# Kernel tuning notes

Hardware: AMD Instinct MI355X
Metric: run time of the kernel (lower is better)

The kernel has to match this reference:

```python
import jax, jax.numpy as jnp
import numpy as np

B, F, N, S, D = 128, 3, 64, 96, 64  # batch, features, nodes, steps, d_model
DIN = F + 1  # delta_t channel appended inside forward


def _layer_norm(x, g, b, eps=1e-5):
    mu = jnp.mean(x, -1, keepdims=True)
    var = jnp.mean((x - mu) ** 2, -1, keepdims=True)
    return (x - mu) * jax.lax.rsqrt(var + eps) * g + b


def _encoder_layer(x, inw, inb, ow, ob, w1, b1, w2, b2, g1, be1, g2, be2):
    # x: (B, N, D). Torch post-norm TransformerEncoderLayer, nhead=1, eval mode (no dropout).
    q, k, v = jnp.split(x @ inw.T + inb, 3, axis=-1)
    scores = jnp.einsum('bnd,bmd->bnm', q, k) / jnp.sqrt(jnp.asarray(D, x.dtype))
    a = jnp.einsum('bnm,bmd->bnd', jax.nn.softmax(scores, -1), v) @ ow.T + ob
    x = _layer_norm(x + a, g1, be1)
    ff = jax.nn.relu(x @ w1.T + b1) @ w2.T + b2
    return _layer_norm(x + ff, g2, be2)


def _diff_conv(x, adj, w, b):
    x1 = jnp.einsum('bcv,wv->bcw', x, adj)
    x2 = jnp.einsum('bcv,wv->bcw', x1, adj)
    z = jnp.concatenate([x, x1, x2], axis=1)  # (B, 3C, N)
    return jnp.einsum('bcn,oc->bon', z, w) + b[None, :, None]


def _forward(x, adj, h0, tp, uw, ub, cw, cb):
    times = x[:, 2, 0, :]  # (B, S) timestamps
    dt = jnp.concatenate([jnp.zeros((B, 1), x.dtype), times[:, 1:] - times[:, :-1]], axis=1)  # (B, S)
    xs = (jnp.transpose(x, (3, 0, 1, 2)), jnp.transpose(dt)[:, :, None])  # (S,B,F,N), (S,B,1)

    def step(h, inp):
        xt, d = inp  # (B,F,N), (B,1)
        xin = jnp.concatenate([xt, jnp.broadcast_to(d[:, :, None], (B, 1, N))], axis=1)  # (B,DIN,N)
        y = jnp.transpose(h, (0, 2, 1))  # (B, N, D): nodes are the attention sequence
        for i in range(2):
            y = _encoder_layer(y, *(a[i] for a in tp))
        eps = jnp.transpose(y, (0, 2, 1))  # (B, D, N)
        hd = jnp.sqrt(1.0 - d)[:, :, None] * h - jnp.sqrt(d)[:, :, None] * eps
        xg = jnp.concatenate([xin, hd], axis=1)  # (B, DIN+D, N)
        u = jax.nn.sigmoid(_diff_conv(xg, adj, uw, ub))
        c = jnp.tanh(_diff_conv(xg, adj, cw, cb))
        hn = u * hd + (1.0 - u) * c
        return hn, hn

    _, outs = jax.lax.scan(step, h0, xs)  # (S, B, D, N)
    return jnp.transpose(outs, (1, 3, 2, 0))  # (B, N, D, S) == stack().permute(1,3,2,0)


def setup_inputs() -> dict:
    key = jax.random.key(0)
    ks = jax.random.split(key, 12)
    s = 0.05
    x = jax.random.normal(ks[0], (B, F, N, S), jnp.float32)
    inc = jax.random.uniform(ks[1], (B, S), jnp.float32, 0.001, 0.01)
    x = x.at[:, 2, 0, :].set(jnp.cumsum(inc, axis=1))  # monotone times, delta_t in (0, 0.01)
    adj = jax.random.uniform(ks[2], (N, N), jnp.float32)
    adj = adj / jnp.sum(adj, axis=1, keepdims=True)
    h0 = jax.random.normal(ks[3], (B, D, N), jnp.float32)
    lengths = jax.random.randint(ks[4], (B,), 1, S, jnp.int32)  # unused by forward
    return {
        'x': x, 'adj': adj, 'lengths': lengths, 'h0': h0,
        't_inw': jax.random.normal(ks[5], (2, 3 * D, D), jnp.float32) * s,
        't_inb': jnp.zeros((2, 3 * D), jnp.float32),
        't_ow': jax.random.normal(ks[6], (2, D, D), jnp.float32) * s,
        't_ob': jnp.zeros((2, D), jnp.float32),
        't_w1': jax.random.normal(ks[7], (2, 64, D), jnp.float32) * s,
        't_b1': jnp.zeros((2, 64), jnp.float32),
        't_w2': jax.random.normal(ks[8], (2, D, 64), jnp.float32) * s,
        't_b2': jnp.zeros((2, D), jnp.float32),
        't_g1': jnp.ones((2, D), jnp.float32), 't_be1': jnp.zeros((2, D), jnp.float32),
        't_g2': jnp.ones((2, D), jnp.float32), 't_be2': jnp.zeros((2, D), jnp.float32),
        'uw': jax.random.normal(ks[9], (D, 3 * (DIN + D)), jnp.float32) * s,
        'ub': jnp.zeros((D,), jnp.float32),
        'cw': jax.random.normal(ks[10], (D, 3 * (DIN + D)), jnp.float32) * s,
        'cb': jnp.zeros((D,), jnp.float32),
    }


def reference(x, adj, lengths, h0, t_inw, t_inb, t_ow, t_ob, t_w1, t_b1, t_w2, t_b2,
              t_g1, t_be1, t_g2, t_be2, uw, ub, cw, cb):
    tp = (t_inw, t_inb, t_ow, t_ob, t_w1, t_b1, t_w2, t_b2, t_g1, t_be1, t_g2, t_be2)
    return _forward(x, adj, h0, tp, uw, ub, cw, cb)
```

## Files before the change

### kernel.cpp

```cpp
#include <hip/hip_runtime.h>
#include <math.h>

#define TPB 512

typedef __attribute__((ext_vector_type(8))) short bf16x8;
typedef __attribute__((ext_vector_type(4))) float f32x4;
typedef unsigned short u16;

#define MFMA(a, b, c) __builtin_amdgcn_mfma_f32_16x16x32_bf16(a, b, c, 0, 0, 0)

__device__ __forceinline__ u16 f2bf(float f) {
  union { float f; unsigned u; } v; v.f = f;
  unsigned u = v.u;
  return (u16)((u + 0x7fffu + ((u >> 16) & 1u)) >> 16);
}
__device__ __forceinline__ float bf2f(u16 h) {
  union { unsigned u; float f; } v; v.u = ((unsigned)h) << 16; return v.f;
}
__device__ __forceinline__ unsigned cvt2(float a0, float a1) {
  return (unsigned)f2bf(a0) | ((unsigned)f2bf(a1) << 16);
}
__device__ __forceinline__ void cvt4u(float a0, float a1, float a2, float a3, u16 o[4]) {
  o[0] = f2bf(a0); o[1] = f2bf(a1); o[2] = f2bf(a2); o[3] = f2bf(a3);
}
// ... 12 lines not shown
}
template<int PREW>
__device__ __forceinline__ bf16x8 wfrag(const float* __restrict__ Wg,
                                        const u16* __restrict__ Wp,
                                        int m, int f, int kh, int lane) {
  if constexpr (PREW)
    return *(const bf16x8*)(Wp + (size_t)m * 4096 + f * 1024 + kh * 512 + lane * 8);
  else
    return fragG(Wg, f * 16, 64, kh * 32, lane);
}

__global__ __launch_bounds__(256)
void prep_kernel(const float* __restrict__ t_inw, const float* __restrict__ t_ow,
                 const float* __restrict__ t_w1, const float* __restrict__ t_w2,
                 const float* __restrict__ adj, const float* __restrict__ x,
                 u16* __restrict__ wp, float* __restrict__ adj2,
                 float* __restrict__ wsDT, u16* __restrict__ wsX, int doX) {
  int m = blockIdx.x;
  if (m == 12) {
    for (int e = threadIdx.x; e < 4096; e += 256) {
      int w = e >> 6, u = e & 63;
      float sum = 0.f;
      for (int v = 0; v < 64; ++v) sum += adj[w * 64 + v] * adj[v * 64 + u];
      adj2[e] = sum;
    }
    return;
  }
  if (m >= 13) {
    if (!doX) return;
    int b = m - 13;
    const float* times = x + ((size_t)b * 3 + 2) * 64 * 96;
    for (int i = threadIdx.x; i < 96 * 256; i += 256) {
      int s = i >> 8, idx = i & 255, f = idx >> 6, n = idx & 63;
      float v;
      if (f < 3) v = x[(((size_t)b * 3 + f) * 64 + n) * 96 + s];
      else {
        float dt = s ? (times[s] - times[s - 1]) : 0.f;
        v = dt;
        if (n == 0) wsDT[b * 96 + s] = dt;
      }
      wsX[((size_t)b * 96 + s) * 256 + idx] = f2bf(v);
    }
    return;
  }
  int l = m / 6, r = m % 6;
  const float* W;
  if (r < 3)       W = t_inw + l * 12288 + r * 4096;
  else if (r == 3) W = t_ow + l * 4096;
  else if (r == 4) W = t_w1 + l * 4096;
  else             W = t_w2 + l * 4096;
  for (int t = threadIdx.x; t < 4096; t += 256) {
    int j = t & 7, ln = (t >> 3) & 63, kh = (t >> 9) & 1, f = t >> 10;
    int row = f * 16 + (ln & 15);
    int k = kh * 32 + ((ln >> 4) << 3) + j;
    wp[(size_t)m * 4096 + t] = f2bf(W[row * 64 + k]);
  }
}

template<int PREW>
__global__ __launch_bounds__(TPB, 2)
void gcrnn_kernel(const float* __restrict__ x,
                  const float* __restrict__ adj,
                  const float* __restrict__ h0,
                  const float* __restrict__ t_inw, const float* __restrict__ t_inb,
                  const float* __restrict__ t_ow,  const float* __restrict__ t_ob,
                  const float* __restrict__ t_w1,  const float* __restrict__ t_b1,
                  const float* __restrict__ t_w2,  const float* __restrict__ t_b2,
                  const float* __restrict__ t_g1,  const float* __restrict__ t_be1,
                  const float* __restrict__ t_g2,  const float* __restrict__ t_be2,
                  const float* __restrict__ uw,    const float* __restrict__ ub,
                  const float* __restrict__ cw,    const float* __restrict__ cb,
                  const u16* __restrict__ wsW,
                  const float* __restrict__ adj2g,
                  const float* __restrict__ wsDT,
                  const u16* __restrict__ wsX,
                  float* __restrict__ wsOut,
                  float* __restrict__ out,
                  int useStage, int useXT)
{
  const int b = blockIdx.x;
  const int tid = threadIdx.x;
  const int wv = tid >> 6;
  const int lane = tid & 63;
  const int lx = lane & 15;
  const int gq = (lane >> 4) << 2;
  const int rs = wv & 3;
  const int of0 = (wv >> 2) * 2;
  const int fA = wv >> 2;

  __shared__ __align__(16) u16 adjB[64 * 72];
  __shared__ __align__(16) u16 adj2B[64 * 72];
  __shared__ __align__(16) u16 ysB[64 * 72];
  __shared__ __align__(16) u16 pool[4 * 4608];
  __shared__ __align__(16) u16 zTB[64 * 232];
  __shared__ __align__(16) u16 uwcwB[2 * 4 * 7 * 512];

  u16* Qb  = pool;
  u16* Kb  = pool + 4608;
  u16* VTb = pool + 9216;
  u16* Pb  = pool + 13824;
  u16* xgB = pool;

  float hreg[2][4];
  {
    const int nb = rs * 16 + gq;
#pragma unroll
    for (int ff = 0; ff < 2; ++ff) {
      int o = (of0 + ff) * 16 + lx;
      float4 hv = *(const float4*)(h0 + (size_t)b * 4096 + o * 64 + nb);
#pragma unroll
      for (int j = 0; j < 4; ++j) {
        hreg[ff][j] = (&hv.x)[j];
        ysB[(nb + j) * 72 + o] = f2bf(hreg[ff][j]);
      }
    }
  }
  for (int i = tid; i < 4096; i += TPB)
    adjB[(i >> 6) * 72 + (i & 63)] = f2bf(adj[i]);
  if constexpr (PREW) {
    for (int i = tid; i < 4096; i += TPB)
      adj2B[(i >> 6) * 72 + (i & 63)] = f2bf(adj2g[i]);
  } else {
    for (int i = tid; i < 4096; i += TPB) {
      int w = i >> 6, u = i & 63;
      float sum = 0.f;
      for (int v = 0; v < 64; ++v) sum += adj[w * 64 + v] * adj[v * 64 + u];
      adj2B[w * 72 + u] = f2bf(sum);
    }
  }
  for (int i = tid; i < 2 * 4 * 7 * 512; i += TPB) {
    int t = i;
    int j = t & 7; t >>= 3;
    int ln = t & 63; t >>= 6;
    int kh = t % 7; t /= 7;
    int f = t & 3; int mat = t >> 2;
    int o = f * 16 + (ln & 15);
    int k = kh * 32 + ((ln >> 4) << 3) + j;
    const float* W = mat ? cw : uw;
    uwcwB[i] = (k < 204) ? f2bf(W[o * 204 + k]) : (u16)0;
  }
  for (int i = tid; i < 64 * 28; i += TPB)
    zTB[(i / 28) * 232 + 204 + (i % 28)] = 0;
  __syncthreads();

  const float* times = x + ((size_t)b * 3 + 2) * 64 * 96;
  float hdreg[2][4];

  for (int s = 0; s < 96; ++s) {
    float dcur = useXT ? wsDT[b * 96 + s]
                       : ((s == 0) ? 0.f : (times[s] - times[s - 1]));
    float sq1 = sqrtf(1.f - dcur), sq2 = sqrtf(dcur);

    for (int l = 0; l < 2; ++l) {
      const int l6 = l * 6;
      const float* inw = t_inw + l * 12288;
      const float* inb = t_inb + l * 192;
      const float* ow  = t_ow  + l * 4096;
      const float* ob  = t_ob  + l * 64;
      const float* w1  = t_w1  + l * 4096;
      const float* bb1 = t_b1  + l * 64;
      const float* w2  = t_w2  + l * 4096;
      const float* bb2 = t_b2  + l * 64;
      const float* g1  = t_g1  + l * 64;
      const float* be1 = t_be1 + l * 64;
      const float* g2  = t_g2  + l * 64;
      const float* be2 = t_be2 + l * 64;

      bf16x8 fq[2][2], fk[2][2], fw1r[2][2], fvr[2];
#pragma unroll
      for (int fi = 0; fi < 2; ++fi)
#pragma unroll
        for (int kh = 0; kh < 2; ++kh) {
          fq[fi][kh]   = wfrag<PREW>(inw,        wsW, l6 + 0, fA + fi * 2, kh, lane);
          fk[fi][kh]   = wfrag<PREW>(inw + 4096, wsW, l6 + 1, fA + fi * 2, kh, lane);
          fw1r[fi][kh] = wfrag<PREW>(w1,         wsW, l6 + 4, fA + fi * 2, kh, lane);
        }
      if (wv >= 4) {
#pragma unroll
        for (int kh = 0; kh < 2; ++kh)
          fvr[kh] = wfrag<PREW>(inw + 8192, wsW, l6 + 2, rs, kh, lane);
      }

      {
        bf16x8 a0 = fragL(ysB, rs * 16, 72, 0, lane);
        bf16x8 a1 = fragL(ysB, rs * 16, 72, 32, lane);
#pragma unroll
        for (int fi = 0; fi < 2; ++fi) {
          int f = fA + fi * 2;
          int col = f * 16 + lx;
          {
            f32x4 acc = {0.f, 0.f, 0.f, 0.f};
            acc = MFMA(a0, fq[fi][0], acc);
            acc = MFMA(a1, fq[fi][1], acc);
            float bv = inb[col];
            u16 o4[4]; cvt4u(acc[0] + bv, acc[1] + bv, acc[2] + bv, acc[3] + bv, o4);
#pragma unroll
            for (int j = 0; j < 4; ++j)
              Qb[(rs * 16 + gq + j) * 72 + col] = o4[j];
          }
          {
// ... 35 lines not shown
          for (int f = 0; f < 4; ++f) { float e = __expf(sc[f][j] - m1); sc[f][j] = e; s1 += e; }
          s1 += __shfl_xor(s1, 1); s1 += __shfl_xor(s1, 2);
          s1 += __shfl_xor(s1, 4); s1 += __shfl_xor(s1, 8);
          float inv = 1.f / s1;
          int row = rs * 16 + gq + j;
          u16 o4[4];
          cvt4u(sc[0][j] * inv, sc[1][j] * inv, sc[2][j] * inv, sc[3][j] * inv, o4);
#pragma unroll
          for (int f = 0; f < 4; ++f)
            Pb[row * 72 + f * 16 + lx] = o4[f];
        }
      } else {
#pragma unroll
        for (int f = 0; f < 4; ++f) {
          f32x4 acc = {0.f, 0.f, 0.f, 0.f};
          acc = MFMA(fvr[0], fragL(ysB, f * 16, 72, 0, lane), acc);
          acc = MFMA(fvr[1], fragL(ysB, f * 16, 72, 32, lane), acc);
          int dd0 = rs * 16 + gq;
          u16 o4[4];
          cvt4u(acc[0] + inb[128 + dd0], acc[1] + inb[128 + dd0 + 1],
                acc[2] + inb[128 + dd0 + 2], acc[3] + inb[128 + dd0 + 3], o4);
#pragma unroll
          for (int j = 0; j < 4; ++j)
            VTb[(dd0 + j) * 72 + f * 16 + lx] = o4[j];
        }
      }
      __syncthreads();

      bf16x8 fo[4][2];
      if (wv < 4) {
#pragma unroll
        for (int f = 0; f < 4; ++f)
#pragma unroll
          for (int kh = 0; kh < 2; ++kh)
            fo[f][kh] = wfrag<PREW>(ow, wsW, l6 + 3, f, kh, lane);
      }
      {
        bf16x8 pa0 = fragL(Pb, rs * 16, 72, 0, lane);
        bf16x8 pa1 = fragL(Pb, rs * 16, 72, 32, lane);
#pragma unroll
        for (int fi = 0; fi < 2; ++fi) {
          int f = fA + fi * 2;
          f32x4 acc = {0.f, 0.f, 0.f, 0.f};
          acc = MFMA(pa0, fragL(VTb, f * 16, 72, 0, lane), acc);
          acc = MFMA(pa1, fragL(VTb, f * 16, 72, 32, lane), acc);
          u16 o4[4]; cvt4u(acc[0], acc[1], acc[2], acc[3], o4);
#pragma unroll
          for (int j = 0; j < 4; ++j)
            Qb[(rs * 16 + gq + j) * 72 + f * 16 + lx] = o4[j];
        }
// ... 2 lines not shown

      if (wv < 4) {
        bf16x8 a0 = fragL(Qb, rs * 16, 72, 0, lane);
        bf16x8 a1 = fragL(Qb, rs * 16, 72, 32, lane);
        float t4[4][4];
#pragma unroll
        for (int f = 0; f < 4; ++f) {
          f32x4 acc = {0.f, 0.f, 0.f, 0.f};
          acc = MFMA(a0, fo[f][0], acc);
          acc = MFMA(a1, fo[f][1], acc);
          int col = f * 16 + lx;
          float bv = ob[col];
#pragma unroll
          for (int j = 0; j < 4; ++j) {
            int row = rs * 16 + gq + j;
            t4[f][j] = acc[j] + bv + bf2f(ysB[row * 72 + col]);
          }
        }
#pragma unroll
        for (int j = 0; j < 4; ++j) {
          float s1 = t4[0][j] + t4[1][j] + t4[2][j] + t4[3][j];
          float s2 = t4[0][j] * t4[0][j] + t4[1][j] * t4[1][j]
                   + t4[2][j] * t4[2][j] + t4[3][j] * t4[3][j];
          s1 += __shfl_xor(s1, 1); s2 += __shfl_xor(s2, 1);
          s1 += __shfl_xor(s1, 2); s2 += __shfl_xor(s2, 2);
          s1 += __shfl_xor(s1, 4); s2 += __shfl_xor(s2, 4);
          s1 += __shfl_xor(s1, 8); s2 += __shfl_xor(s2, 8);
          float mu = s1 * 0.015625f;
          float rstd = rsqrtf(s2 * 0.015625f - mu * mu + 1e-5f);
          int row = rs * 16 + gq + j;
          u16 o4[4];
          cvt4u((t4[0][j] - mu) * rstd * g1[0 * 16 + lx] + be1[0 * 16 + lx],
                (t4[1][j] - mu) * rstd * g1[1 * 16 + lx] + be1[1 * 16 + lx],
                (t4[2][j] - mu) * rstd * g1[2 * 16 + lx] + be1[2 * 16 + lx],
                (t4[3][j] - mu) * rstd * g1[3 * 16 + lx] + be1[3 * 16 + lx], o4);
#pragma unroll
          for (int f = 0; f < 4; ++f)
            ysB[row * 72 + f * 16 + lx] = o4[f];
        }
      }
      __syncthreads();

      bf16x8 fw2[4][2];
      if (wv < 4) {
#pragma unroll
        for (int f = 0; f < 4; ++f)
#pragma unroll
          for (int kh = 0; kh < 2; ++kh)
            fw2[f][kh] = wfrag<PREW>(w2, wsW, l6 + 5, f, kh, lane);
      }
      {
        bf16x8 a0 = fragL(ysB, rs * 16, 72, 0, lane);
        bf16x8 a1 = fragL(ysB, rs * 16, 72, 32, lane);
#pragma unroll
        for (int fi = 0; fi < 2; ++fi) {
          int f = fA + fi * 2;
          f32x4 acc = {0.f, 0.f, 0.f, 0.f};
          acc = MFMA(a0, fw1r[fi][0], acc);
          acc = MFMA(a1, fw1r[fi][1], acc);
          int col = f * 16 + lx;
          float bv = bb1[col];
          u16 o4[4];
          cvt4u(fmaxf(acc[0] + bv, 0.f), fmaxf(acc[1] + bv, 0.f),
                fmaxf(acc[2] + bv, 0.f), fmaxf(acc[3] + bv, 0.f), o4);
#pragma unroll
          for (int j = 0; j < 4; ++j)
            Kb[(rs * 16 + gq + j) * 72 + col] = o4[j];
        }
      }
      __syncthreads();

      if (wv < 4) {
        bf16x8 a0 = fragL(Kb, rs * 16, 72, 0, lane);
        bf16x8 a1 = fragL(Kb, rs * 16, 72, 32, lane);
        float t4[4][4];
#pragma unroll
        for (int f = 0; f < 4; ++f) {
          f32x4 acc = {0.f, 0.f, 0.f, 0.f};
          acc = MFMA(a0, fw2[f][0], acc);
          acc = MFMA(a1, fw2[f][1], acc);
          int col = f * 16 + lx;
          float bv = bb2[col];
#pragma unroll
          for (int j = 0; j < 4; ++j) {
            int row = rs * 16 + gq + j;
            t4[f][j] = acc[j] + bv + bf2f(ysB[row * 72 + col]);
          }
        }
#pragma unroll
        for (int j = 0; j < 4; ++j) {
          float s1 = t4[0][j] + t4[1][j] + t4[2][j] + t4[3][j];
          float s2 = t4[0][j] * t4[0][j] + t4[1][j] * t4[1][j]
                   + t4[2][j] * t4[2][j] + t4[3][j] * t4[3][j];
          s1 += __shfl_xor(s1, 1); s2 += __shfl_xor(s2, 1);
          s1 += __shfl_xor(s1, 2); s2 += __shfl_xor(s2, 2);
// ... 4 lines not shown
          int row = rs * 16 + gq + j;
          u16 o4[4];
          cvt4u((t4[0][j] - mu) * rstd * g2[0 * 16 + lx] + be2[0 * 16 + lx],
                (t4[1][j] - mu) * rstd * g2[1 * 16 + lx] + be2[1 * 16 + lx],
                (t4[2][j] - mu) * rstd * g2[2 * 16 + lx] + be2[2 * 16 + lx],
                (t4[3][j] - mu) * rstd * g2[3 * 16 + lx] + be2[3 * 16 + lx], o4);
#pragma unroll
          for (int f = 0; f < 4; ++f)
            ysB[row * 72 + f * 16 + lx] = o4[f];
        }
      }
      __syncthreads();
    }

    {
      if (useXT) {
        const u16* xr = wsX + ((size_t)b * 96 + s) * 256;
        for (int i = tid; i < 256; i += TPB) {
          u16 v = xr[i];
          int f = i >> 6, n = i & 63;
          xgB[f * 72 + n] = v;
          zTB[n * 232 + f] = v;
        }
      } else {
        for (int i = tid; i < 256; i += TPB) {
          int f = i >> 6, n = i & 63;
          float v = (f < 3) ? x[(((size_t)b * 3 + f) * 64 + n) * 96 + s] : dcur;
          u16 v16 = f2bf(v);
          xgB[f * 72 + n] = v16;
          zTB[n * 232 + f] = v16;
        }
      }
      const int nb = rs * 16 + gq;
#pragma unroll
      for (int ff = 0; ff < 2; ++ff) {
        int o = (of0 + ff) * 16 + lx;
        float hd0 = sq1 * hreg[ff][0] - sq2 * bf2f(ysB[(nb + 0) * 72 + o]);
        float hd1 = sq1 * hreg[ff][1] - sq2 * bf2f(ysB[(nb + 1) * 72 + o]);
        float hd2 = sq1 * hreg[ff][2] - sq2 * bf2f(ysB[(nb + 2) * 72 + o]);
        float hd3 = sq1 * hreg[ff][3] - sq2 * bf2f(ysB[(nb + 3) * 72 + o]);
        hdreg[ff][0] = hd0; hdreg[ff][1] = hd1; hdreg[ff][2] = hd2; hdreg[ff][3] = hd3;
        unsigned p0 = cvt2(hd0, hd1), p1 = cvt2(hd2, hd3);
        zTB[(nb + 0) * 232 + 4 + o] = (u16)p0;
        zTB[(nb + 1) * 232 + 4 + o] = (u16)(p0 >> 16);
        zTB[(nb + 2) * 232 + 4 + o] = (u16)p1;
        zTB[(nb + 3) * 232 + 4 + o] = (u16)(p1 >> 16);
// ... 46 lines not shown
        for (int j = 0; j < 4; ++j) {
          float u = 1.f / (1.f + __expf(-(aU[ff][j] + bu_)));
          float z = aC[ff][j] + bc_;
          z = fminf(fmaxf(z, -15.f), 15.f);
          float e2 = __expf(2.f * z);
          float cval = (e2 - 1.f) / (e2 + 1.f);
          float hn = u * hdreg[ff][j] + (1.f - u) * cval;
          hreg[ff][j] = hn;
          (&ov.x)[j] = hn;
        }
        unsigned pk0 = cvt2(ov.x, ov.y), pk1 = cvt2(ov.z, ov.w);
        ysB[(nb + 0) * 72 + o] = (u16)pk0;
        ysB[(nb + 1) * 72 + o] = (u16)(pk0 >> 16);
        ysB[(nb + 2) * 72 + o] = (u16)pk1;
        ysB[(nb + 3) * 72 + o] = (u16)(pk1 >> 16);
        if (useStage) {
          *(float4*)(wsOut + ((size_t)b * 96 + s) * 4096 + o * 64 + nb) = ov;
        } else {
#pragma unroll
          for (int j = 0; j < 4; ++j)
            out[((size_t)(b * 64 + (nb + j)) * 64 + o) * 96 + s] = (&ov.x)[j];
        }
      }
    }
    __syncthreads();
  }
}

__global__ __launch_bounds__(256)
void transp_kernel(const float* __restrict__ ws, float* __restrict__ out) {
  int blk = blockIdx.x;
  int b = blk >> 6, o = blk & 63;
  __shared__ float t[96 * 68];
  for (int i = threadIdx.x; i < 96 * 64; i += 256) {
    int ss = i >> 6, n = i & 63;
    t[ss * 68 + n] = ws[((size_t)b * 96 + ss) * 4096 + o * 64 + n];
  }
// ... 18 lines not shown
  const float* t_ob  = (const float*)d_in[7];
  const float* t_w1  = (const float*)d_in[8];
  const float* t_b1  = (const float*)d_in[9];
  const float* t_w2  = (const float*)d_in[10];
  const float* t_b2  = (const float*)d_in[11];
  const float* t_g1  = (const float*)d_in[12];
  const float* t_be1 = (const float*)d_in[13];
  const float* t_g2  = (const float*)d_in[14];
  const float* t_be2 = (const float*)d_in[15];
  const float* uw    = (const float*)d_in[16];
  const float* ub    = (const float*)d_in[17];
  const float* cw    = (const float*)d_in[18];
  const float* cb    = (const float*)d_in[19];
  float* out = (float*)d_out;

  const size_t offAdj2 = 98304;
  const size_t offDT   = 114688;
  const size_t offX    = 163840;
  const size_t offStageFull = 6455296;
  const size_t stageBytes = (size_t)128 * 96 * 4096 * 4;

  int prew = 0, useStage = 0, useXT = 0;
  size_t stageOff = 0;
  if (ws_size >= offStageFull + stageBytes) { prew = 1; useXT = 1; useStage = 1; stageOff = offStageFull; }
  else if (ws_size >= offX + stageBytes)    { prew = 1; useStage = 1; stageOff = offX; }
  else if (ws_size >= stageBytes)           { useStage = 1; }
  else if (ws_size >= offX)                 { prew = 1; }

  u16*   wsW   = (u16*)d_ws;
  float* adj2g = (float*)((char*)d_ws + offAdj2);
  float* wsDT  = (float*)((char*)d_ws + offDT);
  u16*   wsX   = (u16*)((char*)d_ws + offX);
  float* wsOut = (float*)((char*)d_ws + stageOff);

  if (prew)
    hipLaunchKernelGGL(prep_kernel, dim3(13 + (useXT ? 128 : 0)), dim3(256), 0, stream,
                       t_inw, t_ow, t_w1, t_w2, adj, x, wsW, adj2g, wsDT, wsX, useXT);

  if (prew)
    hipLaunchKernelGGL(gcrnn_kernel<1>, dim3(128), dim3(TPB), 0, stream,
                       x, adj, h0, t_inw, t_inb, t_ow, t_ob, t_w1, t_b1,
                       t_w2, t_b2, t_g1, t_be1, t_g2, t_be2, uw, ub, cw, cb,
                       wsW, adj2g, wsDT, wsX, wsOut, out, useStage, useXT);
  else
    hipLaunchKernelGGL(gcrnn_kernel<0>, dim3(128), dim3(TPB), 0, stream,
                       x, adj, h0, t_inw, t_inb, t_ow, t_ob, t_w1, t_b1,
                       t_w2, t_b2, t_g1, t_be1, t_g2, t_be2, uw, ub, cw, cb,
                       wsW, adj2g, wsDT, wsX, wsOut, out, useStage, 0);

  if (useStage)
    hipLaunchKernelGGL(transp_kernel, dim3(128 * 64), dim3(256), 0, stream, wsOut, out);
}
```

Measured before the change: 1.599 ms.

## Split fast path with double-buffered LDS, fused FFN/diffusion stages and pre-swizzled adj²

Splits the kernel into a fast path, used when workspace is large enough, and a separate fallback kernel. The fast path gives Q/K/V/P/xg their own LDS buffers and ping-pongs the layer input between Y0 and Y1 to remove aliasing. It also folds the last layer's FFN/LayerNorm epilogue straight into the hd/xg build, and interleaves the first diffusion hops with the gate MFMAs. adj² is precomputed and pre-swizzled into MFMA fragment layout in global memory, and biases are hoisted out of the step loop. The aim is fewer barriers and less per-step LDS/global traffic, at the cost of more LDS and register pressure, which may reduce occupancy.

```diff
diff --git a/kernel.cpp b/kernel.cpp
--- a/kernel.cpp
+++ b/kernel.cpp
@@ -50,20 +50,27 @@
 void prep_kernel(const float* __restrict__ t_inw, const float* __restrict__ t_ow,
                  const float* __restrict__ t_w1, const float* __restrict__ t_w2,
                  const float* __restrict__ adj, const float* __restrict__ x,
-                 u16* __restrict__ wp, float* __restrict__ adj2,
-                 float* __restrict__ wsDT, u16* __restrict__ wsX, int doX) {
+                 u16* __restrict__ wp, u16* __restrict__ wpA2,
+                 float* __restrict__ wsDT, u16* __restrict__ wsX) {
   int m = blockIdx.x;
   if (m == 12) {
+    __shared__ float a2[4096];
     for (int e = threadIdx.x; e < 4096; e += 256) {
       int w = e >> 6, u = e & 63;
       float sum = 0.f;
       for (int v = 0; v < 64; ++v) sum += adj[w * 64 + v] * adj[v * 64 + u];
-      adj2[e] = sum;
+      a2[e] = sum;
+    }
+    __syncthreads();
+    for (int t = threadIdx.x; t < 4096; t += 256) {
+      int j = t & 7, ln = (t >> 3) & 63, kh = (t >> 9) & 1, f = t >> 10;
+      int row = f * 16 + (ln & 15);
+      int k = kh * 32 + ((ln >> 4) << 3) + j;
+      wpA2[t] = f2bf(a2[row * 64 + k]);
     }
     return;
   }
   if (m >= 13) {
-    if (!doX) return;
     int b = m - 13;
     const float* times = x + ((size_t)b * 3 + 2) * 64 * 96;
     for (int i = threadIdx.x; i < 96 * 256; i += 256) {
@@ -93,26 +100,18 @@
   }
 }
 
-template<int PREW>
 __global__ __launch_bounds__(TPB, 2)
-void gcrnn_kernel(const float* __restrict__ x,
-                  const float* __restrict__ adj,
-                  const float* __restrict__ h0,
-                  const float* __restrict__ t_inw, const float* __restrict__ t_inb,
-                  const float* __restrict__ t_ow,  const float* __restrict__ t_ob,
-                  const float* __restrict__ t_w1,  const float* __restrict__ t_b1,
-                  const float* __restrict__ t_w2,  const float* __restrict__ t_b2,
-                  const float* __restrict__ t_g1,  const float* __restrict__ t_be1,
-                  const float* __restrict__ t_g2,  const float* __restrict__ t_be2,
-                  const float* __restrict__ uw,    const float* __restrict__ ub,
-                  const float* __restrict__ cw,    const float* __restrict__ cb,
-                  const u16* __restrict__ wsW,
-                  const float* __restrict__ adj2g,
-                  const float* __restrict__ wsDT,
-                  const u16* __restrict__ wsX,
-                  float* __restrict__ wsOut,
-                  float* __restrict__ out,
-                  int useStage, int useXT)
+void gcrnn_fast(const float* __restrict__ adj,
+                const float* __restrict__ h0,
+                const float* __restrict__ t_inb, const float* __restrict__ t_ob,
+                const float* __restrict__ t_b1,  const float* __restrict__ t_b2,
+                const float* __restrict__ t_g1,  const float* __restrict__ t_be1,
+                const float* __restrict__ t_g2,  const float* __restrict__ t_be2,
+                const float* __restrict__ uw,    const float* __restrict__ ub,
+                const float* __restrict__ cw,    const float* __restrict__ cb,
+                const u16* __restrict__ wsW,  const u16* __restrict__ wsA2,
+                const float* __restrict__ wsDT, const u16* __restrict__ wsX,
+                float* __restrict__ wsOut)
 {
   const int b = blockIdx.x;
   const int tid = threadIdx.x;
@@ -125,17 +124,15 @@
   const int fA = wv >> 2;
 
   __shared__ __align__(16) u16 adjB[64 * 72];
-  __shared__ __align__(16) u16 adj2B[64 * 72];
-  __shared__ __align__(16) u16 ysB[64 * 72];
-  __shared__ __align__(16) u16 pool[4 * 4608];
+  __shared__ __align__(16) u16 Y0[64 * 72];
+  __shared__ __align__(16) u16 Y1[64 * 72];
+  __shared__ __align__(16) u16 Qb[64 * 72];
+  __shared__ __align__(16) u16 Kb[64 * 72];
+  __shared__ __align__(16) u16 VTb[64 * 72];
+  __shared__ __align__(16) u16 Pb[64 * 72];
+  __shared__ __align__(16) u16 xgB[80 * 72];
   __shared__ __align__(16) u16 zTB[64 * 232];
   __shared__ __align__(16) u16 uwcwB[2 * 4 * 7 * 512];
-
-  u16* Qb  = pool;
-  u16* Kb  = pool + 4608;
-  u16* VTb = pool + 9216;
-  u16* Pb  = pool + 13824;
-  u16* xgB = pool;
 
   float hreg[2][4];
   {
@@ -147,23 +144,12 @@
 #pragma unroll
       for (int j = 0; j < 4; ++j) {
         hreg[ff][j] = (&hv.x)[j];
-        ysB[(nb + j) * 72 + o] = f2bf(hreg[ff][j]);
+        Y0[(nb + j) * 72 + o] = f2bf(hreg[ff][j]);
       }
     }
   }
   for (int i = tid; i < 4096; i += TPB)
     adjB[(i >> 6) * 72 + (i & 63)] = f2bf(adj[i]);
-  if constexpr (PREW) {
-    for (int i = tid; i < 4096; i += TPB)
-      adj2B[(i >> 6) * 72 + (i & 63)] = f2bf(adj2g[i]);
-  } else {
-    for (int i = tid; i < 4096; i += TPB) {
-      int w = i >> 6, u = i & 63;
-      float sum = 0.f;
-      for (int v = 0; v < 64; ++v) sum += adj[w * 64 + v] * adj[v * 64 + u];
-      adj2B[w * 72 + u] = f2bf(sum);
-    }
-  }
   for (int i = tid; i < 2 * 4 * 7 * 512; i += TPB) {
     int t = i;
     int j = t & 7; t >>= 3;
@@ -177,25 +163,23 @@
   }
   for (int i = tid; i < 64 * 28; i += TPB)
     zTB[(i / 28) * 232 + 204 + (i % 28)] = 0;
+  for (int i = tid; i < 12 * 72; i += TPB)
+    xgB[68 * 72 + i] = 0;
   __syncthreads();
 
-  const float* times = x + ((size_t)b * 3 + 2) * 64 * 96;
+  const float buo = ub[of0 * 16 + lx], buo2 = ub[(of0 + 1) * 16 + lx];
+  const float bco = cb[of0 * 16 + lx], bco2 = cb[(of0 + 1) * 16 + lx];
   float hdreg[2][4];
 
   for (int s = 0; s < 96; ++s) {
-    float dcur = useXT ? wsDT[b * 96 + s]
-                       : ((s == 0) ? 0.f : (times[s] - times[s - 1]));
+    float dcur = wsDT[b * 96 + s];
     float sq1 = sqrtf(1.f - dcur), sq2 = sqrtf(dcur);
 
     for (int l = 0; l < 2; ++l) {
       const int l6 = l * 6;
-      const float* inw = t_inw + l * 12288;
       const float* inb = t_inb + l * 192;
-      const float* ow  = t_ow  + l * 4096;
       const float* ob  = t_ob  + l * 64;
-      const float* w1  = t_w1  + l * 4096;
       const float* bb1 = t_b1  + l * 64;
-      const float* w2  = t_w2  + l * 4096;
       const float* bb2 = t_b2  + l * 64;
       const float* g1  = t_g1  + l * 64;
       const float* be1 = t_be1 + l * 64;
@@ -207,19 +191,19 @@
       for (int fi = 0; fi < 2; ++fi)
 #pragma unroll
         for (int kh = 0; kh < 2; ++kh) {
-          fq[fi][kh]   = wfrag<PREW>(inw,        wsW, l6 + 0, fA + fi * 2, kh, lane);
-          fk[fi][kh]   = wfrag<PREW>(inw + 4096, wsW, l6 + 1, fA + fi * 2, kh, lane);
-          fw1r[fi][kh] = wfrag<PREW>(w1,         wsW, l6 + 4, fA + fi * 2, kh, lane);
+          fq[fi][kh]   = wfrag<1>(nullptr, wsW, l6 + 0, fA + fi * 2, kh, lane);
+          fk[fi][kh]   = wfrag<1>(nullptr, wsW, l6 + 1, fA + fi * 2, kh, lane);
+          fw1r[fi][kh] = wfrag<1>(nullptr, wsW, l6 + 4, fA + fi * 2, kh, lane);
         }
       if (wv >= 4) {
 #pragma unroll
         for (int kh = 0; kh < 2; ++kh)
-          fvr[kh] = wfrag<PREW>(inw + 8192, wsW, l6 + 2, rs, kh, lane);
+          fvr[kh] = wfrag<1>(nullptr, wsW, l6 + 2, rs, kh, lane);
       }
 
       {
-        bf16x8 a0 = fragL(ysB, rs * 16, 72, 0, lane);
-        bf16x8 a1 = fragL(ysB, rs * 16, 72, 32, lane);
+        bf16x8 a0 = fragL(Y0, rs * 16, 72, 0, lane);
+        bf16x8 a1 = fragL(Y0, rs * 16, 72, 32, lane);
 #pragma unroll
         for (int fi = 0; fi < 2; ++fi) {
           int f = fA + fi * 2;
@@ -285,8 +269,8 @@
 #pragma unroll
         for (int f = 0; f < 4; ++f) {
           f32x4 acc = {0.f, 0.f, 0.f, 0.f};
-          acc = MFMA(fvr[0], fragL(ysB, f * 16, 72, 0, lane), acc);
-          acc = MFMA(fvr[1], fragL(ysB, f * 16, 72, 32, lane), acc);
+          acc = MFMA(fvr[0], fragL(Y0, f * 16, 72, 0, lane), acc);
+          acc = MFMA(fvr[1], fragL(Y0, f * 16, 72, 32, lane), acc);
           int dd0 = rs * 16 + gq;
           u16 o4[4];
           cvt4u(acc[0] + inb[128 + dd0], acc[1] + inb[128 + dd0 + 1],
@@ -304,7 +288,7 @@
         for (int f = 0; f < 4; ++f)
 #pragma unroll
           for (int kh = 0; kh < 2; ++kh)
-            fo[f][kh] = wfrag<PREW>(ow, wsW, l6 + 3, f, kh, lane);
+            fo[f][kh] = wfrag<1>(nullptr, wsW, l6 + 3, f, kh, lane);
       }
       {
         bf16x8 pa0 = fragL(Pb, rs * 16, 72, 0, lane);
@@ -337,7 +321,7 @@
 #pragma unroll
           for (int j = 0; j < 4; ++j) {
             int row = rs * 16 + gq + j;
-            t4[f][j] = acc[j] + bv + bf2f(ysB[row * 72 + col]);
+            t4[f][j] = acc[j] + bv + bf2f(Y0[row * 72 + col]);
           }
         }
 #pragma unroll
@@ -359,22 +343,20 @@
                 (t4[3][j] - mu) * rstd * g1[3 * 16 + lx] + be1[3 * 16 + lx], o4);
 #pragma unroll
           for (int f = 0; f < 4; ++f)
-            ysB[row * 72 + f * 16 + lx] = o4[f];
+            Y1[row * 72 + f * 16 + lx] = o4[f];
         }
       }
       __syncthreads();
 
       bf16x8 fw2[4][2];
-      if (wv < 4) {
-#pragma unroll
-        for (int f = 0; f < 4; ++f)
-#pragma unroll
-          for (int kh = 0; kh < 2; ++kh)
-            fw2[f][kh] = wfrag<PREW>(w2, wsW, l6 + 5, f, kh, lane);
-      }
+#pragma unroll
+      for (int f = 0; f < 4; ++f)
+#pragma unroll
+        for (int kh = 0; kh < 2; ++kh)
+          fw2[f][kh] = wfrag<1>(nullptr, wsW, l6 + 5, f, kh, lane);
       {
-        bf16x8 a0 = fragL(ysB, rs * 16, 72, 0, lane);
-        bf16x8 a1 = fragL(ysB, rs * 16, 72, 32, lane);
+        bf16x8 a0 = fragL(Y1, rs * 16, 72, 0, lane);
+        bf16x8 a1 = fragL(Y1, rs * 16, 72, 32, lane);
 #pragma unroll
         for (int fi = 0; fi < 2; ++fi) {
           int f = fA + fi * 2;
@@ -393,6 +375,461 @@
       }
       __syncthreads();
 
+      if (l == 0) {
+        if (wv < 4) {
+          bf16x8 a0 = fragL(Kb, rs * 16, 72, 0, lane);
+          bf16x8 a1 = fragL(Kb, rs * 16, 72, 32, lane);
+          float t4[4][4];
+#pragma unroll
+          for (int f = 0; f < 4; ++f) {
+            f32x4 acc = {0.f, 0.f, 0.f, 0.f};
+            acc = MFMA(a0, fw2[f][0], acc);
+            acc = MFMA(a1, fw2[f][1], acc);
+            int col = f * 16 + lx;
+            float bv = bb2[col];
+#pragma unroll
+            for (int j = 0; j < 4; ++j) {
+              int row = rs * 16 + gq + j;
+              t4[f][j] = acc[j] + bv + bf2f(Y1[row * 72 + col]);
+            }
+          }
+#pragma unroll
+          for (int j = 0; j < 4; ++j) {
+            float s1 = t4[0][j] + t4[1][j] + t4[2][j] + t4[3][j];
+            float s2 = t4[0][j] * t4[0][j] + t4[1][j] * t4[1][j]
+                     + t4[2][j] * t4[2][j] + t4[3][j] * t4[3][j];
+            s1 += __shfl_xor(s1, 1); s2 += __shfl_xor(s2, 1);
+            s1 += __shfl_xor(s1, 2); s2 += __shfl_xor(s2, 2);
+            s1 += __shfl_xor(s1, 4); s2 += __shfl_xor(s2, 4);
+            s1 += __shfl_xor(s1, 8); s2 += __shfl_xor(s2, 8);
+            float mu = s1 * 0.015625f;
+            float rstd = rsqrtf(s2 * 0.015625f - mu * mu + 1e-5f);
+            int row = rs * 16 + gq + j;
+            u16 o4[4];
+            cvt4u((t4[0][j] - mu) * rstd * g2[0 * 16 + lx] + be2[0 * 16 + lx],
+                  (t4[1][j] - mu) * rstd * g2[1 * 16 + lx] + be2[1 * 16 + lx],
+                  (t4[2][j] - mu) * rstd * g2[2 * 16 + lx] + be2[2 * 16 + lx],
+                  (t4[3][j] - mu) * rstd * g2[3 * 16 + lx] + be2[3 * 16 + lx], o4);
+#pragma unroll
+            for (int f = 0; f < 4; ++f)
+              Y0[row * 72 + f * 16 + lx] = o4[f];
+          }
+        }
+      } else {
+        bf16x8 a0 = fragL(Kb, rs * 16, 72, 0, lane);
+        bf16x8 a1 = fragL(Kb, rs * 16, 72, 32, lane);
+        float t4[4][4];
+#pragma unroll
+        for (int f = 0; f < 4; ++f) {
+          f32x4 acc = {0.f, 0.f, 0.f, 0.f};
+          acc = MFMA(a0, fw2[f][0], acc);
+          acc = MFMA(a1, fw2[f][1], acc);
+          int col = f * 16 + lx;
+          float bv = bb2[col];
+#pragma unroll
+          for (int j = 0; j < 4; ++j) {
+            int row = rs * 16 + gq + j;
+            t4[f][j] = acc[j] + bv + bf2f(Y1[row * 72 + col]);
+          }
+        }
+#pragma unroll
+        for (int j = 0; j < 4; ++j) {
+          float s1 = t4[0][j] + t4[1][j] + t4[2][j] + t4[3][j];
+          float s2 = t4[0][j] * t4[0][j] + t4[1][j] * t4[1][j]
+                   + t4[2][j] * t4[2][j] + t4[3][j] * t4[3][j];
+          s1 += __shfl_xor(s1, 1); s2 += __shfl_xor(s2, 1);
+          s1 += __shfl_xor(s1, 2); s2 += __shfl_xor(s2, 2);
+          s1 += __shfl_xor(s1, 4); s2 += __shfl_xor(s2, 4);
+          s1 += __shfl_xor(s1, 8); s2 += __shfl_xor(s2, 8);
+          float mu = s1 * 0.015625f;
+          float rstd = rsqrtf(s2 * 0.015625f - mu * mu + 1e-5f);
+#pragma unroll
+          for (int f = 0; f < 4; ++f) {
+            int col = f * 16 + lx;
+            t4[f][j] = (t4[f][j] - mu) * rstd * g2[col] + be2[col];
+          }
+        }
+        {
+          const u16* xr = wsX + ((size_t)b * 96 + s) * 256;
+          for (int i = tid; i < 256; i += TPB) {
+            u16 v = xr[i];
+            int f = i >> 6, n = i & 63;
+            xgB[f * 72 + n] = v;
+            zTB[n * 232 + f] = v;
+          }
+        }
+        const int nb = rs * 16 + gq;
+#pragma unroll
+        for (int f = 0; f < 4; ++f) {
+          if ((f >> 1) == (wv >> 2)) {
+            const int ff = f & 1;
+            int o = f * 16 + lx;
+            float hd0 = sq1 * hreg[ff][0] - sq2 * t4[f][0];
+            float hd1 = sq1 * hreg[ff][1] - sq2 * t4[f][1];
+            float hd2 = sq1 * hreg[ff][2] - sq2 * t4[f][2];
+            float hd3 = sq1 * hreg[ff][3] - sq2 * t4[f][3];
+            hdreg[ff][0] = hd0; hdreg[ff][1] = hd1;
+            hdreg[ff][2] = hd2; hdreg[ff][3] = hd3;
+            unsigned p0 = cvt2(hd0, hd1), p1 = cvt2(hd2, hd3);
+            zTB[(nb + 0) * 232 + 4 + o] = (u16)p0;
+            zTB[(nb + 1) * 232 + 4 + o] = (u16)(p0 >> 16);
+            zTB[(nb + 2) * 232 + 4 + o] = (u16)p1;
+            zTB[(nb + 3) * 232 + 4 + o] = (u16)(p1 >> 16);
+            uint2 pk; pk.x = p0; pk.y = p1;
+            *(uint2*)(xgB + (4 + o) * 72 + nb) = pk;
+          }
+        }
+      }
+      __syncthreads();
+    }
+
+    f32x4 aU0 = {0.f,0.f,0.f,0.f}, aU1 = {0.f,0.f,0.f,0.f};
+    f32x4 aC0 = {0.f,0.f,0.f,0.f}, aC1 = {0.f,0.f,0.f,0.f};
+    {
+      bf16x8 g0 = *(const bf16x8*)(wsA2 + rs * 1024 + lane * 8);
+      bf16x8 g1 = *(const bf16x8*)(wsA2 + rs * 1024 + 512 + lane * 8);
+      bf16x8 aj0 = fragL(adjB, rs * 16, 72, 0, lane);
+      bf16x8 aj1 = fragL(adjB, rs * 16, 72, 32, lane);
+
+#define HT(A0, A1, CF, OFF) { \
+      f32x4 acc = {0.f,0.f,0.f,0.f}; \
+      acc = MFMA(A0, fragL(xgB, (CF) * 16, 72, 0, lane), acc); \
+      acc = MFMA(A1, fragL(xgB, (CF) * 16, 72, 32, lane), acc); \
+      int c = (CF) * 16 + lx; \
+      if (c < 68) { u16 o4[4]; cvt4u(acc[0], acc[1], acc[2], acc[3], o4); \
+        _Pragma("unroll") for (int j = 0; j < 4; ++j) \
+          zTB[(rs * 16 + gq + j) * 232 + (OFF) + c] = o4[j]; } }
+
+#define J01 { _Pragma("unroll") for (int kh = 0; kh < 2; ++kh) { \
+      bf16x8 a = fragL(zTB, rs * 16, 232, kh * 32, lane); \
+      { const u16* pu = uwcwB + (size_t)((of0 + 0) * 7 + kh) * 512 + lane * 8; \
+        const u16* pc = uwcwB + (size_t)((4 + of0 + 0) * 7 + kh) * 512 + lane * 8; \
+        aU0 = MFMA(a, *(const bf16x8*)pu, aU0); \
+        aC0 = MFMA(a, *(const bf16x8*)pc, aC0); } \
+      { const u16* pu = uwcwB + (size_t)((of0 + 1) * 7 + kh) * 512 + lane * 8; \
+        const u16* pc = uwcwB + (size_t)((4 + of0 + 1) * 7 + kh) * 512 + lane * 8; \
+        aU1 = MFMA(a, *(const bf16x8*)pu, aU1); \
+        aC1 = MFMA(a, *(const bf16x8*)pc, aC1); } } }
+
+      if (wv < 4) {
+        HT(aj0, aj1, 0, 68); HT(aj0, aj1, 2, 68); HT(aj0, aj1, 4, 68);
+        J01;
+        HT(g0, g1, 1, 136); HT(g0, g1, 3, 136);
+      } else {
+        HT(aj0, aj1, 1, 68); HT(aj0, aj1, 3, 68);
+        J01;
+        HT(g0, g1, 0, 136); HT(g0, g1, 2, 136); HT(g0, g1, 4, 136);
+      }
+#undef HT
+#undef J01
+    }
+    __syncthreads();
+
+    {
+#pragma unroll
+      for (int kh = 2; kh < 7; ++kh) {
+        bf16x8 a = fragL(zTB, rs * 16, 232, kh * 32, lane);
+        {
+          const u16* pu = uwcwB + (size_t)((of0 + 0) * 7 + kh) * 512 + lane * 8;
+          const u16* pc = uwcwB + (size_t)((4 + of0 + 0) * 7 + kh) * 512 + lane * 8;
+          aU0 = MFMA(a, *(const bf16x8*)pu, aU0);
+          aC0 = MFMA(a, *(const bf16x8*)pc, aC0);
+        }
+        {
+          const u16* pu = uwcwB + (size_t)((of0 + 1) * 7 + kh) * 512 + lane * 8;
+          const u16* pc = uwcwB + (size_t)((4 + of0 + 1) * 7 + kh) * 512 + lane * 8;
+          aU1 = MFMA(a, *(const bf16x8*)pu, aU1);
+          aC1 = MFMA(a, *(const bf16x8*)pc, aC1);
+        }
+      }
+      const int nb = rs * 16 + gq;
+#pragma unroll
+      for (int ff = 0; ff < 2; ++ff) {
+        f32x4 aU = ff ? aU1 : aU0;
+        f32x4 aC = ff ? aC1 : aC0;
+        float bu_ = ff ? buo2 : buo;
+        float bc_ = ff ? bco2 : bco;
+        int o = (of0 + ff) * 16 + lx;
+        float4 ov;
+#pragma unroll
+        for (int j = 0; j < 4; ++j) {
+          float u = 1.f / (1.f + __expf(-(aU[j] + bu_)));
+          float z = aC[j] + bc_;
+          z = fminf(fmaxf(z, -15.f), 15.f);
+          float e2 = __expf(2.f * z);
+          float cval = (e2 - 1.f) / (e2 + 1.f);
+          float hn = u * hdreg[ff][j] + (1.f - u) * cval;
+          hreg[ff][j] = hn;
+          (&ov.x)[j] = hn;
+        }
+        unsigned pk0 = cvt2(ov.x, ov.y), pk1 = cvt2(ov.z, ov.w);
+        Y0[(nb + 0) * 72 + o] = (u16)pk0;
+        Y0[(nb + 1) * 72 + o] = (u16)(pk0 >> 16);
+        Y0[(nb + 2) * 72 + o] = (u16)pk1;
+        Y0[(nb + 3) * 72 + o] = (u16)(pk1 >> 16);
+        *(float4*)(wsOut + ((size_t)b * 96 + s) * 4096 + o * 64 + nb) = ov;
+      }
+    }
+    __syncthreads();
+  }
+}
+
+__global__ __launch_bounds__(TPB, 2)
+void gcrnn_fb(const float* __restrict__ x, const float* __restrict__ adj,
+              const float* __restrict__ h0,
+              const float* __restrict__ t_inw, const float* __restrict__ t_inb,
+              const float* __restrict__ t_ow,  const float* __restrict__ t_ob,
+              const float* __restrict__ t_w1,  const float* __restrict__ t_b1,
+              const float* __restrict__ t_w2,  const float* __restrict__ t_b2,
+              const float* __restrict__ t_g1,  const float* __restrict__ t_be1,
+              const float* __restrict__ t_g2,  const float* __restrict__ t_be2,
+              const float* __restrict__ uw,    const float* __restrict__ ub,
+              const float* __restrict__ cw,    const float* __restrict__ cb,
+              float* __restrict__ out)
+{
+  const int b = blockIdx.x;
+  const int tid = threadIdx.x;
+  const int wv = tid >> 6;
+  const int lane = tid & 63;
+  const int lx = lane & 15;
+  const int gq = (lane >> 4) << 2;
+  const int rs = wv & 3;
+  const int of0 = (wv >> 2) * 2;
+  const int fA = wv >> 2;
+
+  __shared__ __align__(16) u16 adjB[64 * 72];
+  __shared__ __align__(16) u16 adj2B[64 * 72];
+  __shared__ __align__(16) u16 ysB[64 * 72];
+  __shared__ __align__(16) u16 pool[4 * 4608];
+  __shared__ __align__(16) u16 zTB[64 * 232];
+  __shared__ __align__(16) u16 uwcwB[2 * 4 * 7 * 512];
+
+  u16* Qb  = pool;
+  u16* Kb  = pool + 4608;
+  u16* VTb = pool + 9216;
+  u16* Pb  = pool + 13824;
+  u16* xgB = pool;
+
+  float hreg[2][4];
+  {
+    const int nb = rs * 16 + gq;
+#pragma unroll
+    for (int ff = 0; ff < 2; ++ff) {
+      int o = (of0 + ff) * 16 + lx;
+      float4 hv = *(const float4*)(h0 + (size_t)b * 4096 + o * 64 + nb);
+#pragma unroll
+      for (int j = 0; j < 4; ++j) {
+        hreg[ff][j] = (&hv.x)[j];
+        ysB[(nb + j) * 72 + o] = f2bf(hreg[ff][j]);
+      }
+    }
+  }
+  for (int i = tid; i < 4096; i += TPB)
+    adjB[(i >> 6) * 72 + (i & 63)] = f2bf(adj[i]);
+  for (int i = tid; i < 4096; i += TPB) {
+    int w = i >> 6, u = i & 63;
+    float sum = 0.f;
+    for (int v = 0; v < 64; ++v) sum += adj[w * 64 + v] * adj[v * 64 + u];
+    adj2B[w * 72 + u] = f2bf(sum);
+  }
+  for (int i = tid; i < 2 * 4 * 7 * 512; i += TPB) {
+    int t = i;
+    int j = t & 7; t >>= 3;
+    int ln = t & 63; t >>= 6;
+    int kh = t % 7; t /= 7;
+    int f = t & 3; int mat = t >> 2;
+    int o = f * 16 + (ln & 15);
+    int k = kh * 32 + ((ln >> 4) << 3) + j;
+    const float* W = mat ? cw : uw;
+    uwcwB[i] = (k < 204) ? f2bf(W[o * 204 + k]) : (u16)0;
+  }
+  for (int i = tid; i < 64 * 28; i += TPB)
+    zTB[(i / 28) * 232 + 204 + (i % 28)] = 0;
+  __syncthreads();
+
+  const float* times = x + ((size_t)b * 3 + 2) * 64 * 96;
+  float hdreg[2][4];
+
+  for (int s = 0; s < 96; ++s) {
+    float dcur = (s == 0) ? 0.f : (times[s] - times[s - 1]);
+    float sq1 = sqrtf(1.f - dcur), sq2 = sqrtf(dcur);
+
+    for (int l = 0; l < 2; ++l) {
+      const float* inw = t_inw + l * 12288;
+      const float* inb = t_inb + l * 192;
+      const float* ow  = t_ow  + l * 4096;
+      const float* ob  = t_ob  + l * 64;
+      const float* w1  = t_w1  + l * 4096;
+      const float* bb1 = t_b1  + l * 64;
+      const float* w2  = t_w2  + l * 4096;
+      const float* bb2 = t_b2  + l * 64;
+      const float* g1  = t_g1  + l * 64;
+      const float* be1 = t_be1 + l * 64;
+      const float* g2  = t_g2  + l * 64;
+      const float* be2 = t_be2 + l * 64;
+
+      {
+        bf16x8 a0 = fragL(ysB, rs * 16, 72, 0, lane);
+        bf16x8 a1 = fragL(ysB, rs * 16, 72, 32, lane);
+#pragma unroll
+        for (int fi = 0; fi < 2; ++fi) {
+          int f = fA + fi * 2;
+          int col = f * 16 + lx;
+          {
+            f32x4 acc = {0.f, 0.f, 0.f, 0.f};
+            acc = MFMA(a0, fragG(inw, f * 16, 64, 0, lane), acc);
+            acc = MFMA(a1, fragG(inw, f * 16, 64, 32, lane), acc);
+            float bv = inb[col];
+            u16 o4[4]; cvt4u(acc[0] + bv, acc[1] + bv, acc[2] + bv, acc[3] + bv, o4);
+#pragma unroll
+            for (int j = 0; j < 4; ++j)
+              Qb[(rs * 16 + gq + j) * 72 + col] = o4[j];
+          }
+          {
+            f32x4 acc = {0.f, 0.f, 0.f, 0.f};
+            acc = MFMA(a0, fragG(inw + 4096, f * 16, 64, 0, lane), acc);
+            acc = MFMA(a1, fragG(inw + 4096, f * 16, 64, 32, lane), acc);
+            float bv = inb[64 + col];
+            u16 o4[4]; cvt4u(acc[0] + bv, acc[1] + bv, acc[2] + bv, acc[3] + bv, o4);
+#pragma unroll
+            for (int j = 0; j < 4; ++j)
+              Kb[(rs * 16 + gq + j) * 72 + col] = o4[j];
+          }
+        }
+      }
+      __syncthreads();
+
+      if (wv < 4) {
+        bf16x8 qa0 = fragL(Qb, rs * 16, 72, 0, lane);
+        bf16x8 qa1 = fragL(Qb, rs * 16, 72, 32, lane);
+        f32x4 sc[4];
+#pragma unroll
+        for (int f = 0; f < 4; ++f) {
+          f32x4 acc = {0.f, 0.f, 0.f, 0.f};
+          acc = MFMA(qa0, fragL(Kb, f * 16, 72, 0, lane), acc);
+          acc = MFMA(qa1, fragL(Kb, f * 16, 72, 32, lane), acc);
+#pragma unroll
+          for (int j = 0; j < 4; ++j) acc[j] *= 0.125f;
+          sc[f] = acc;
+        }
+#pragma unroll
+        for (int j = 0; j < 4; ++j) {
+          float m1 = fmaxf(fmaxf(sc[0][j], sc[1][j]), fmaxf(sc[2][j], sc[3][j]));
+          m1 = fmaxf(m1, __shfl_xor(m1, 1));
+          m1 = fmaxf(m1, __shfl_xor(m1, 2));
+          m1 = fmaxf(m1, __shfl_xor(m1, 4));
+          m1 = fmaxf(m1, __shfl_xor(m1, 8));
+          float s1 = 0.f;
+#pragma unroll
+          for (int f = 0; f < 4; ++f) { float e = __expf(sc[f][j] - m1); sc[f][j] = e; s1 += e; }
+          s1 += __shfl_xor(s1, 1); s1 += __shfl_xor(s1, 2);
+          s1 += __shfl_xor(s1, 4); s1 += __shfl_xor(s1, 8);
+          float inv = 1.f / s1;
+          int row = rs * 16 + gq + j;
+          u16 o4[4];
+          cvt4u(sc[0][j] * inv, sc[1][j] * inv, sc[2][j] * inv, sc[3][j] * inv, o4);
+#pragma unroll
+          for (int f = 0; f < 4; ++f)
+            Pb[row * 72 + f * 16 + lx] = o4[f];
+        }
+      } else {
+        bf16x8 wa0 = fragG(inw + 8192, rs * 16, 64, 0, lane);
+        bf16x8 wa1 = fragG(inw + 8192, rs * 16, 64, 32, lane);
+#pragma unroll
+        for (int f = 0; f < 4; ++f) {
+          f32x4 acc = {0.f, 0.f, 0.f, 0.f};
+          acc = MFMA(wa0, fragL(ysB, f * 16, 72, 0, lane), acc);
+          acc = MFMA(wa1, fragL(ysB, f * 16, 72, 32, lane), acc);
+          int dd0 = rs * 16 + gq;
+          u16 o4[4];
+          cvt4u(acc[0] + inb[128 + dd0], acc[1] + inb[128 + dd0 + 1],
+                acc[2] + inb[128 + dd0 + 2], acc[3] + inb[128 + dd0 + 3], o4);
+#pragma unroll
+          for (int j = 0; j < 4; ++j)
+            VTb[(dd0 + j) * 72 + f * 16 + lx] = o4[j];
+        }
+      }
+      __syncthreads();
+
+      {
+        bf16x8 pa0 = fragL(Pb, rs * 16, 72, 0, lane);
+        bf16x8 pa1 = fragL(Pb, rs * 16, 72, 32, lane);
+#pragma unroll
+        for (int fi = 0; fi < 2; ++fi) {
+          int f = fA + fi * 2;
+          f32x4 acc = {0.f, 0.f, 0.f, 0.f};
+          acc = MFMA(pa0, fragL(VTb, f * 16, 72, 0, lane), acc);
+          acc = MFMA(pa1, fragL(VTb, f * 16, 72, 32, lane), acc);
+          u16 o4[4]; cvt4u(acc[0], acc[1], acc[2], acc[3], o4);
+#pragma unroll
+          for (int j = 0; j < 4; ++j)
+            Qb[(rs * 16 + gq + j) * 72 + f * 16 + lx] = o4[j];
+        }
+      }
+      __syncthreads();
+
+      if (wv < 4) {
+        bf16x8 a0 = fragL(Qb, rs * 16, 72, 0, lane);
+        bf16x8 a1 = fragL(Qb, rs * 16, 72, 32, lane);
+        float t4[4][4];
+#pragma unroll
+        for (int f = 0; f < 4; ++f) {
+          f32x4 acc = {0.f, 0.f, 0.f, 0.f};
+          acc = MFMA(a0, fragG(ow, f * 16, 64, 0, lane), acc);
+          acc = MFMA(a1, fragG(ow, f * 16, 64, 32, lane), acc);
+          int col = f * 16 + lx;
+          float bv = ob[col];
+#pragma unroll
+          for (int j = 0; j < 4; ++j) {
+            int row = rs * 16 + gq + j;
+            t4[f][j] = acc[j] + bv + bf2f(ysB[row * 72 + col]);
+          }
+        }
+#pragma unroll
+        for (int j = 0; j < 4; ++j) {
+          float s1 = t4[0][j] + t4[1][j] + t4[2][j] + t4[3][j];
+          float s2 = t4[0][j] * t4[0][j] + t4[1][j] * t4[1][j]
+                   + t4[2][j] * t4[2][j] + t4[3][j] * t4[3][j];
+          s1 += __shfl_xor(s1, 1); s2 += __shfl_xor(s2, 1);
+          s1 += __shfl_xor(s1, 2); s2 += __shfl_xor(s2, 2);
+          s1 += __shfl_xor(s1, 4); s2 += __shfl_xor(s2, 4);
+          s1 += __shfl_xor(s1, 8); s2 += __shfl_xor(s2, 8);
+          float mu = s1 * 0.015625f;
+          float rstd = rsqrtf(s2 * 0.015625f - mu * mu + 1e-5f);
+          int row = rs * 16 + gq + j;
+          u16 o4[4];
+          cvt4u((t4[0][j] - mu) * rstd * g1[0 * 16 + lx] + be1[0 * 16 + lx],
+                (t4[1][j] - mu) * rstd * g1[1 * 16 + lx] + be1[1 * 16 + lx],
+                (t4[2][j] - mu) * rstd * g1[2 * 16 + lx] + be1[2 * 16 + lx],
+                (t4[3][j] - mu) * rstd * g1[3 * 16 + lx] + be1[3 * 16 + lx], o4);
+#pragma unroll
+          for (int f = 0; f < 4; ++f)
+            ysB[row * 72 + f * 16 + lx] = o4[f];
+        }
+      }
+      __syncthreads();
+
+      {
+        bf16x8 a0 = fragL(ysB, rs * 16, 72, 0, lane);
+        bf16x8 a1 = fragL(ysB, rs * 16, 72, 32, lane);
+#pragma unroll
+        for (int fi = 0; fi < 2; ++fi) {
+          int f = fA + fi * 2;
+          f32x4 acc = {0.f, 0.f, 0.f, 0.f};
+          acc = MFMA(a0, fragG(w1, f * 16, 64, 0, lane), acc);
+          acc = MFMA(a1, fragG(w1, f * 16, 64, 32, lane), acc);
+          int col = f * 16 + lx;
+          float bv = bb1[col];
+          u16 o4[4];
+          cvt4u(fmaxf(acc[0] + bv, 0.f), fmaxf(acc[1] + bv, 0.f),
+                fmaxf(acc[2] + bv, 0.f), fmaxf(acc[3] + bv, 0.f), o4);
+#pragma unroll
+          for (int j = 0; j < 4; ++j)
+            Kb[(rs * 16 + gq + j) * 72 + col] = o4[j];
+        }
+      }
+      __syncthreads();
+
       if (wv < 4) {
         bf16x8 a0 = fragL(Kb, rs * 16, 72, 0, lane);
         bf16x8 a1 = fragL(Kb, rs * 16, 72, 32, lane);
@@ -400,8 +837,8 @@
 #pragma unroll
         for (int f = 0; f < 4; ++f) {
           f32x4 acc = {0.f, 0.f, 0.f, 0.f};
-          acc = MFMA(a0, fw2[f][0], acc);
-          acc = MFMA(a1, fw2[f][1], acc);
+          acc = MFMA(a0, fragG(w2, f * 16, 64, 0, lane), acc);
+          acc = MFMA(a1, fragG(w2, f * 16, 64, 32, lane), acc);
           int col = f * 16 + lx;
           float bv = bb2[col];
 #pragma unroll
@@ -436,22 +873,12 @@
     }
 
     {
-      if (useXT) {
-        const u16* xr = wsX + ((size_t)b * 96 + s) * 256;
-        for (int i = tid; i < 256; i += TPB) {
-          u16 v = xr[i];
-          int f = i >> 6, n = i & 63;
-          xgB[f * 72 + n] = v;
-          zTB[n * 232 + f] = v;
-        }
-      } else {
-        for (int i = tid; i < 256; i += TPB) {
-          int f = i >> 6, n = i & 63;
-          float v = (f < 3) ? x[(((size_t)b * 3 + f) * 64 + n) * 96 + s] : dcur;
-          u16 v16 = f2bf(v);
-          xgB[f * 72 + n] = v16;
-          zTB[n * 232 + f] = v16;
-        }
+      for (int i = tid; i < 256; i += TPB) {
+        int f = i >> 6, n = i & 63;
+        float v = (f < 3) ? x[(((size_t)b * 3 + f) * 64 + n) * 96 + s] : dcur;
+        u16 v16 = f2bf(v);
+        xgB[f * 72 + n] = v16;
+        zTB[n * 232 + f] = v16;
       }
       const int nb = rs * 16 + gq;
 #pragma unroll
@@ -528,13 +955,9 @@
         ysB[(nb + 1) * 72 + o] = (u16)(pk0 >> 16);
         ysB[(nb + 2) * 72 + o] = (u16)pk1;
         ysB[(nb + 3) * 72 + o] = (u16)(pk1 >> 16);
-        if (useStage) {
-          *(float4*)(wsOut + ((size_t)b * 96 + s) * 4096 + o * 64 + nb) = ov;
-        } else {
-#pragma unroll
-          for (int j = 0; j < 4; ++j)
-            out[((size_t)(b * 64 + (nb + j)) * 64 + o) * 96 + s] = (&ov.x)[j];
-        }
+#pragma unroll
+        for (int j = 0; j < 4; ++j)
+          out[((size_t)(b * 64 + (nb + j)) * 64 + o) * 96 + s] = (&ov.x)[j];
       }
     }
     __syncthreads();
@@ -583,40 +1006,28 @@
   const float* cb    = (const float*)d_in[19];
   float* out = (float*)d_out;
 
-  const size_t offAdj2 = 98304;
-  const size_t offDT   = 114688;
-  const size_t offX    = 163840;
-  const size_t offStageFull = 6455296;
+  const size_t offA2    = 98304;
+  const size_t offDT    = 106496;
+  const size_t offX     = 155648;
+  const size_t offStage = 6447104;
   const size_t stageBytes = (size_t)128 * 96 * 4096 * 4;
 
-  int prew = 0, useStage = 0, useXT = 0;
-  size_t stageOff = 0;
-  if (ws_size >= offStageFull + stageBytes) { prew = 1; useXT = 1; useStage = 1; stageOff = offStageFull; }
-  else if (ws_size >= offX + stageBytes)    { prew = 1; useStage = 1; stageOff = offX; }
-  else if (ws_size >= stageBytes)           { useStage = 1; }
-  else if (ws_size >= offX)                 { prew = 1; }
-
-  u16*   wsW   = (u16*)d_ws;
-  float* adj2g = (float*)((char*)d_ws + offAdj2);
-  float* wsDT  = (float*)((char*)d_ws + offDT);
-  u16*   wsX   = (u16*)((char*)d_ws + offX);
-  float* wsOut = (float*)((char*)d_ws + stageOff);
-
-  if (prew)
-    hipLaunchKernelGGL(prep_kernel, dim3(13 + (useXT ? 128 : 0)), dim3(256), 0, stream,
-                       t_inw, t_ow, t_w1, t_w2, adj, x, wsW, adj2g, wsDT, wsX, useXT);
-
-  if (prew)
-    hipLaunchKernelGGL(gcrnn_kernel<1>, dim3(128), dim3(TPB), 0, stream,
+  if (ws_size >= offStage + stageBytes) {
+    u16*   wsW   = (u16*)d_ws;
+    u16*   wsA2  = (u16*)((char*)d_ws + offA2);
+    float* wsDT  = (float*)((char*)d_ws + offDT);
+    u16*   wsX   = (u16*)((char*)d_ws + offX);
+    float* wsOut = (float*)((char*)d_ws + offStage);
+
+    hipLaunchKernelGGL(prep_kernel, dim3(141), dim3(256), 0, stream,
+                       t_inw, t_ow, t_w1, t_w2, adj, x, wsW, wsA2, wsDT, wsX);
+    hipLaunchKernelGGL(gcrnn_fast, dim3(128), dim3(TPB), 0, stream,
+                       adj, h0, t_inb, t_ob, t_b1, t_b2, t_g1, t_be1, t_g2, t_be2,
+                       uw, ub, cw, cb, wsW, wsA2, wsDT, wsX, wsOut);
+    hipLaunchKernelGGL(transp_kernel, dim3(128 * 64), dim3(256), 0, stream, wsOut, out);
+  } else {
+    hipLaunchKernelGGL(gcrnn_fb, dim3(128), dim3(TPB), 0, stream,
                        x, adj, h0, t_inw, t_inb, t_ow, t_ob, t_w1, t_b1,
-                       t_w2, t_b2, t_g1, t_be1, t_g2, t_be2, uw, ub, cw, cb,
-                       wsW, adj2g, wsDT, wsX, wsOut, out, useStage, useXT);
-  else
-    hipLaunchKernelGGL(gcrnn_kernel<0>, dim3(128), dim3(TPB), 0, stream,
-                       x, adj, h0, t_inw, t_inb, t_ow, t_ob, t_w1, t_b1,
-                       t_w2, t_b2, t_g1, t_be1, t_g2, t_be2, uw, ub, cw, cb,
-                       wsW, adj2g, wsDT, wsX, wsOut, out, useStage, 0);
-
-  if (useStage)
-    hipLaunchKernelGGL(transp_kernel, dim3(128 * 64), dim3(256), 0, stream, wsOut, out);
-}
+                       t_w2, t_b2, t_g1, t_be1, t_g2, t_be2, uw, ub, cw, cb, out);
+  }
+}
```

Result: faster. 1.498 ms (-6.3%).
